# Kernel tuning notes

Measured on AMD Instinct MI355X. Metric: run time of the kernel, lower is better.

Reference implementation:

```python
import jax, jax.numpy as jnp
import numpy as np

B, C, T, HEADS = 4, 1024, 1024, 16


def setup_inputs() -> dict:
    key = jax.random.key(0)
    k0, k1, k2, k3 = jax.random.split(key, 4)
    x = jax.random.normal(k0, (B, C, T), dtype=jnp.float32)
    mask = jax.random.randint(k1, (B, T), 0, 2).astype(bool)  # True = masked position
    scale = 1.0 / np.sqrt(C).astype(np.float32)
    w_kvq = jax.random.normal(k2, (3 * C, C), dtype=jnp.float32) * scale  # Conv1d k=1, no bias
    w_out = jax.random.normal(k3, (C, C), dtype=jnp.float32) * scale
    return {"x": x, "mask": mask, "w_kvq": w_kvq, "w_out": w_out}


def reference(x, mask, w_kvq, w_out):
    b, c, t = x.shape
    h = HEADS
    d = c // h  # head dim; torch scales by sqrt(k.size(1)) = sqrt(d)
    # Conv1d with kernel 1 == per-timestep matmul over channels
    kvq = jnp.einsum('oc,bct->bot', w_kvq, x)  # [B, 3C, T]
    k, v, q = jnp.split(kvq, 3, axis=1)        # each [B, C, T]
    k = k.reshape(b, h, d, t)
    v = v.reshape(b, h, d, t)
    q = q.reshape(b, h, d, t)
    # att[b,h,i,j] = <k_i, q_j> / sqrt(d); i = key pos, j = query pos
    att = jnp.einsum('bhdi,bhdj->bhij', k, q) / jnp.sqrt(jnp.asarray(d, x.dtype))
    # pre-softmax: mask key positions (dim i) with -inf
    att = jnp.where(mask[:, None, :, None], -jnp.inf, att)
    att = jax.nn.softmax(att, axis=2)  # softmax over keys (torch dim=1 of [Bh,Tk,Tq])
    # post-softmax: zero out masked query positions (dim j)
    att = jnp.where(mask[:, None, None, :], jnp.asarray(0.0, x.dtype), att)
    o = jnp.einsum('bhdi,bhij->bhdj', v, att)  # [B, h, d, T]
    o = o.reshape(b, c, t)
    out = x + jnp.einsum('oc,bct->bot', w_out, o)
    # match torch layout: cat over heads along batch dim -> [h*B, T, T]
    att_flat = jnp.transpose(att, (1, 0, 2, 3)).reshape(h * b, t, t)
    return out, att_flat
```

## Files before the change

### kernel.cpp

```cpp
#include <hip/hip_runtime.h>

#define BB 4
#define CC 1024
#define TT 1024
#define HH 16
#define DD 64

typedef __bf16 v8bf __attribute__((ext_vector_type(8)));
typedef __bf16 v4bf __attribute__((ext_vector_type(4)));
typedef float  v4f  __attribute__((ext_vector_type(4)));

__device__ __forceinline__ void async16(const __bf16* g, __bf16* l) {
  __builtin_amdgcn_global_load_lds(
      (const __attribute__((address_space(1))) void*)g,
      (__attribute__((address_space(3))) void*)l, 16, 0, 0);
}

__global__ __launch_bounds__(256) void prep(
    const void* mraw, float* __restrict__ maskf, unsigned int* __restrict__ kmb,
    const float* __restrict__ w_kvq, const float* __restrict__ w_out,
    __bf16* __restrict__ wkb, __bf16* __restrict__ wob,
    const float* __restrict__ x, __bf16* __restrict__ xT)
{
  const int blk = blockIdx.x;
  const int tid = threadIdx.x;
  __shared__ int flagA, flagB;
  __shared__ __bf16 T[64][72];

  if (blk == 0) {
    if (tid == 0) { flagA = 0; flagB = 0; }
    __syncthreads();
    const unsigned char* mb = (const unsigned char*)mraw;
    const int n = BB * TT;
    int a = 0, bfl = 0;
    for (int i = tid; i < n; i += 256) {
      if (mb[i]) { if ((i & 3) == 0) a = 1; else bfl = 1; }
    }
    if (a)   atomicOr(&flagA, 1);
    if (bfl) atomicOr(&flagB, 1);
    __syncthreads();
    int layout;
    if (flagA && !flagB)      layout = 0;
    else if (!flagA && flagB) layout = 1;
    else                      layout = 2;
    const int lane = tid & 63, wave = tid >> 6;
    for (int it = 0; it < 16; it++) {
      int i = it * 256 + tid;
      float m;
      if (layout == 0)      m = (((const int*)mraw)[i]   != 0)   ? 1.f : 0.f;
      else if (layout == 1) m = (((const float*)mraw)[i] != 0.f) ? 1.f : 0.f;
      else                  m = (mb[i] != 0)                     ? 1.f : 0.f;
      maskf[i] = m;
      unsigned long long bal = __ballot(m != 0.f);
      if (lane == 0) {
        int base = (it * 256 + wave * 64) >> 5;
        kmb[base]     = (unsigned int)bal;
        kmb[base + 1] = (unsigned int)(bal >> 32);
      }
    }
  } else if (blk <= 2048) {
    const int cb = blk - 1;
    const float* src; __bf16* dst; int base;
    if (cb < 1536) { src = w_kvq; dst = wkb; base = cb * 2048; }
    else           { src = w_out; dst = wob; base = (cb - 1536) * 2048; }
    int i = base + tid * 8;
    float4 f0 = *(const float4*)(src + i);
    float4 f1 = *(const float4*)(src + i + 4);
    v8bf o;
    o[0] = (__bf16)f0.x; o[1] = (__bf16)f0.y; o[2] = (__bf16)f0.z; o[3] = (__bf16)f0.w;
    o[4] = (__bf16)f1.x; o[5] = (__bf16)f1.y; o[6] = (__bf16)f1.z; o[7] = (__bf16)f1.w;
    *(v8bf*)(dst + i) = o;
  } else {
    const int idx = blk - 2049;
    const int t0 = (idx & 15) * 64, c0 = ((idx >> 4) & 15) * 64, b = idx >> 8;
    {
      int row = tid >> 2, coff = (tid & 3) * 16;
      const float* src = x + ((long)b * CC + c0 + row) * TT + t0 + coff;
#pragma unroll
      for (int s = 0; s < 4; s++) {
        float4 f = *(const float4*)(src + s * 4);
        T[row][coff + s * 4 + 0] = (__bf16)f.x;
        T[row][coff + s * 4 + 1] = (__bf16)f.y;
        T[row][coff + s * 4 + 2] = (__bf16)f.z;
        T[row][coff + s * 4 + 3] = (__bf16)f.w;
      }
    }
    __syncthreads();
    {
      int trow = tid >> 2, ccoff = (tid & 3) * 16;
      __bf16 vals[16];
#pragma unroll
      for (int i = 0; i < 16; i++) vals[i] = T[ccoff + i][trow];
      __bf16* dst = xT + ((long)b * TT + t0 + trow) * CC + c0 + ccoff;
      *(v8bf*)dst       = *(v8bf*)&vals[0];
      *(v8bf*)(dst + 8) = *(v8bf*)&vals[8];
    }
  }
}

__global__ __launch_bounds__(256) void transpose_kq(const __bf16* __restrict__ kvqb,
                                                    __bf16* __restrict__ kqT) {
  const int zz = blockIdx.z;
  const int b = zz >> 1, part = zz & 1;
  const int srcbase = part == 0 ? 0 : 2 * CC;
  const int dstbase = part * CC;
  const int t0 = blockIdx.x * 64, c0 = blockIdx.y * 64;
  __shared__ __bf16 T[64][72];
  const int tid = threadIdx.x;
  {
    int row = tid >> 2, coff = (tid & 3) * 16;
    const __bf16* src = kvqb + ((long)b * 3 * CC + srcbase + c0 + row) * TT + t0 + coff;
    *(v8bf*)&T[row][coff]     = *(const v8bf*)src;
    *(v8bf*)&T[row][coff + 8] = *(const v8bf*)(src + 8);
  }
  __syncthreads();
  {
    int trow = tid >> 2, ccoff = (tid & 3) * 16;
    __bf16 vals[16];
#pragma unroll
    for (int i = 0; i < 16; i++) vals[i] = T[ccoff + i][trow];
    __bf16* dst = kqT + ((long)b * TT + t0 + trow) * (2 * CC) + dstbase + c0 + ccoff;
    *(v8bf*)dst       = *(v8bf*)&vals[0];
    *(v8bf*)(dst + 8) = *(v8bf*)&vals[8];
  }
}

template <int MODE, int NB, int MB>
__global__ __launch_bounds__(256) void gemm_bt(
    const __bf16* __restrict__ A, const __bf16* __restrict__ BTfull,
    const float* __restrict__ Sfull, void* __restrict__ Ofull,
    long strideBT, long strideOS)
{
  constexpr int TOT = NB * MB * BB;
  int flat = blockIdx.x + NB * (blockIdx.y + MB * blockIdx.z);
  int L = (flat & 7) * (TOT / 8) + (flat >> 3);
  const int n0 = (L % NB) * 128;
  const int m0 = ((L / NB) % MB) * 128;
  const int zb = L / (NB * MB);
  const __bf16* BT = BTfull + (long)zb * strideBT;
  __shared__ __align__(16) __bf16 As[128 * 32];
  __shared__ __align__(16) __bf16 Bs[128 * 32];
  const int tid = threadIdx.x;
  const int lane = tid & 63, wave = tid >> 6;
  const int wm = wave >> 1, wn = wave & 1;
  const int ln = lane & 15, q = lane >> 4;

  v4f acc[4][4];
#pragma unroll
  for (int i = 0; i < 4; i++)
#pragma unroll
    for (int j = 0; j < 4; j++) acc[i][j] = (v4f)(0.f);

  const int e0 = tid * 8;
  const int r0 = e0 >> 5, c0 = e0 & 31;
  const int e1 = (256 + tid) * 8;
  const int r1 = e1 >> 5, c1 = e1 & 31;
  const __bf16* ga0 = A  + (long)(m0 + r0) * CC + c0;
  const __bf16* ga1 = A  + (long)(m0 + r1) * CC + c1;
  const __bf16* gb0 = BT + (long)(n0 + r0) * CC + c0;
  const __bf16* gb1 = BT + (long)(n0 + r1) * CC + c1;
  __bf16* lA0 = &As[wave * 512];
  __bf16* lA1 = &As[2048 + wave * 512];
  __bf16* lB0 = &Bs[wave * 512];
  __bf16* lB1 = &Bs[2048 + wave * 512];

  for (int k0 = 0; k0 < CC; k0 += 32) {
    async16(ga0 + k0, lA0);
    async16(ga1 + k0, lA1);
    async16(gb0 + k0, lB0);
    async16(gb1 + k0, lB1);
    __syncthreads();
    v8bf af[4], bfr[4];
#pragma unroll
    for (int mi = 0; mi < 4; mi++)
      af[mi] = *(v8bf*)&As[(wm * 64 + mi * 16 + ln) * 32 + q * 8];
#pragma unroll
    for (int ni = 0; ni < 4; ni++)
      bfr[ni] = *(v8bf*)&Bs[(wn * 64 + ni * 16 + ln) * 32 + q * 8];
#pragma unroll
    for (int mi = 0; mi < 4; mi++)
#pragma unroll
      for (int ni = 0; ni < 4; ni++)
        acc[mi][ni] = __builtin_amdgcn_mfma_f32_16x16x32_bf16(af[mi], bfr[ni], acc[mi][ni], 0, 0, 0);
    __syncthreads();
  }
#pragma unroll
  for (int mi = 0; mi < 4; mi++)
#pragma unroll
    for (int ni = 0; ni < 4; ni++)
#pragma unroll
      for (int r = 0; r < 4; r++) {
        int row = m0 + wm * 64 + mi * 16 + q * 4 + r;
        int col = n0 + wn * 64 + ni * 16 + ln;
        if (MODE == 0) {
          ((__bf16*)Ofull)[(long)zb * strideOS + (long)row * TT + col] = (__bf16)acc[mi][ni][r];
        } else {
          long off = (long)zb * strideOS + (long)row * TT + col;
          ((float*)Ofull)[off] = acc[mi][ni][r] + Sfull[off];
        }
      }
}

__global__ __launch_bounds__(256) void attn_stats(
    const __bf16* __restrict__ kqT, const float* __restrict__ maskf,
    float* __restrict__ psum)
{
  int L = blockIdx.x + 8 * (blockIdx.y + 8 * blockIdx.z);
  L = (L & 7) * 512 + (L >> 3);
  const int jx = L & 7, iy = (L >> 3) & 7, z = L >> 6;
  const int h = z >> 2, b = z & 3;
  const int i0 = iy * 128, j0 = jx * 128;
  const __bf16* kbase = kqT + (long)b * TT * (2 * CC);
  const int tid = threadIdx.x;
  const int lane = tid & 63, wave = tid >> 6;
  const int wi = wave >> 1, wj = wave & 1;
  const int ln = lane & 15, q = lane >> 4;

  v8bf ak[4][2], bq[4][2];
#pragma unroll
  for (int mi = 0; mi < 4; mi++) {
    const __bf16* ar = kbase + (long)(i0 + wi * 64 + mi * 16 + ln) * (2 * CC) + h * DD;
    ak[mi][0] = *(const v8bf*)(ar + q * 8);
    ak[mi][1] = *(const v8bf*)(ar + 32 + q * 8);
  }
#pragma unroll
  for (int ni = 0; ni < 4; ni++) {
    const __bf16* br = kbase + (long)(j0 + wj * 64 + ni * 16 + ln) * (2 * CC) + CC + h * DD;
    bq[ni][0] = *(const v8bf*)(br + q * 8);
    bq[ni][1] = *(const v8bf*)(br + 32 + q * 8);
  }

  v4f acc[4][4];
  __builtin_amdgcn_s_setprio(1);
#pragma unroll
  for (int mi = 0; mi < 4; mi++)
#pragma unroll
    for (int ni = 0; ni < 4; ni++) {
      v4f a = (v4f)(0.f);
      a = __builtin_amdgcn_mfma_f32_16x16x32_bf16(ak[mi][0], bq[ni][0], a, 0, 0, 0);
      a = __builtin_amdgcn_mfma_f32_16x16x32_bf16(ak[mi][1], bq[ni][1], a, 0, 0, 0);
      acc[mi][ni] = a;
    }
  __builtin_amdgcn_s_setprio(0);

  float kmv[4][4];
#pragma unroll
  for (int mi = 0; mi < 4; mi++)
#pragma unroll
    for (int r = 0; r < 4; r++)
      kmv[mi][r] = maskf[b * TT + i0 + wi * 64 + mi * 16 + q * 4 + r];

#pragma unroll
  for (int ni = 0; ni < 4; ni++) {
    float s = 0.f;
#pragma unroll
    for (int mi = 0; mi < 4; mi++)
#pragma unroll
      for (int r = 0; r < 4; r++) {
        float e = (kmv[mi][r] != 0.f) ? 0.f : __expf(acc[mi][ni][r] * 0.125f);
        s += e;
      }
    s += __shfl_xor(s, 16, 64);
    s += __shfl_xor(s, 32, 64);
    if (q == 0) {
      long so = ((long)z * 16 + (i0 >> 6) + wi) * TT + j0 + wj * 64 + ni * 16 + ln;
      psum[so] = s;
    }
  }
}

__global__ __launch_bounds__(256) void gemm_pv(
    const __bf16* __restrict__ kqT, const __bf16* __restrict__ kvqb,
    const float* __restrict__ psum, const float* __restrict__ maskf,
    const unsigned int* __restrict__ kmb,
    float* __restrict__ att, __bf16* __restrict__ oT)
{
  int L = blockIdx.x + 16 * blockIdx.y;
  L = (L & 7) * 128 + (L >> 3);
  const int z = L >> 4, jb = L & 15;
  const int h = z >> 2, b = z & 3;
  const int j0 = jb * 64;
  __shared__ __align__(16) char smem[37376];
  float* stl = (float*)smem;
  unsigned int* kmw = (unsigned int*)(smem + 256);
  const int tid = threadIdx.x;
  const int lane = tid & 63, wave = tid >> 6;
  const int ln = lane & 15, q = lane >> 4;
  __bf16 (*Pt)[72] = (__bf16(*)[72])(smem + 512 + wave * 9216);

  const __bf16* kbase = kqT + (long)b * TT * (2 * CC);
  const __bf16* vbase = kvqb + (long)(b * 3 * CC + CC + h * DD) * TT;

  if (tid < 64) {
    float S = 0.f;
#pragma unroll
    for (int t = 0; t < 16; t++) S += psum[((long)z * 16 + t) * TT + j0 + tid];
    stl[tid] = (maskf[b * TT + j0 + tid] != 0.f) ? 0.f : 1.f / S;
  }
  if (tid < 32) kmw[tid] = kmb[b * 32 + tid];
  __syncthreads();

  v8bf bq[4][2];
#pragma unroll
  for (int ni = 0; ni < 4; ni++) {
    const __bf16* qr = kbase + (long)(j0 + ni * 16 + ln) * (2 * CC) + CC + h * DD;
    bq[ni][0] = *(const v8bf*)(qr + q * 8);
    bq[ni][1] = *(const v8bf*)(qr + 32 + q * 8);
  }
  float stq[4];
#pragma unroll
  for (int ni = 0; ni < 4; ni++) stq[ni] = stl[ni * 16 + ln];

  v4f acc[4][4];
#pragma unroll
  for (int i = 0; i < 4; i++)
#pragma unroll
    for (int j = 0; j < 4; j++) acc[i][j] = (v4f)(0.f);

  for (int it = 0; it < 4; it++) {
    const int ibase = wave * 256 + it * 64;
#pragma unroll
    for (int mi = 0; mi < 4; mi++) {
      const __bf16* arow = kbase + (long)(ibase + mi * 16 + ln) * (2 * CC) + h * DD;
      v8bf ak0 = *(const v8bf*)(arow + q * 8);
      v8bf ak1 = *(const v8bf*)(arow + 32 + q * 8);
#pragma unroll
      for (int ni = 0; ni < 4; ni++) {
        v4f l4 = (v4f)(0.f);
        l4 = __builtin_amdgcn_mfma_f32_16x16x32_bf16(ak0, bq[ni][0], l4, 0, 0, 0);
        l4 = __builtin_amdgcn_mfma_f32_16x16x32_bf16(ak1, bq[ni][1], l4, 0, 0, 0);
        v4bf pb;
#pragma unroll
        for (int r = 0; r < 4; r++) {
          int i_loc = mi * 16 + q * 4 + r;
          int i_glob = ibase + i_loc;
          unsigned int mbit = (kmw[i_glob >> 5] >> (i_glob & 31)) & 1u;
          float p = mbit ? 0.f : __expf(l4[r] * 0.125f) * stq[ni];
          att[((long)z << 20) + (long)i_glob * TT + j0 + ni * 16 + ln] = p;
          pb[r] = (__bf16)p;
        }
        *(v4bf*)&Pt[ni * 16 + ln][mi * 16 + q * 4] = pb;
      }
    }
    v8bf ap[4][2], bv[4][2];
#pragma unroll
    for (int ji = 0; ji < 4; ji++)
#pragma unroll
      for (int ki = 0; ki < 2; ki++)
        ap[ji][ki] = *(v8bf*)&Pt[ji * 16 + ln][ki * 32 + q * 8];
#pragma unroll
    for (int di = 0; di < 4; di++)
#pragma unroll
      for (int ki = 0; ki < 2; ki++)
        bv[di][ki] = *(const v8bf*)(vbase + (long)(di * 16 + ln) * TT + ibase + ki * 32 + q * 8);
    __builtin_amdgcn_s_setprio(1);
#pragma unroll
    for (int ji = 0; ji < 4; ji++)
#pragma unroll
      for (int di = 0; di < 4; di++) {
        acc[ji][di] = __builtin_amdgcn_mfma_f32_16x16x32_bf16(ap[ji][0], bv[di][0], acc[ji][di], 0, 0, 0);
        acc[ji][di] = __builtin_amdgcn_mfma_f32_16x16x32_bf16(ap[ji][1], bv[di][1], acc[ji][di], 0, 0, 0);
      }
    __builtin_amdgcn_s_setprio(0);
  }

  float (*red0)[68] = (float(*)[68])(smem + 512);
  float (*red1)[68] = (float(*)[68])(smem + 512 + 17408);
  __syncthreads();
  if ((wave & 1) == 0) {
    float (*red)[68] = (wave == 0) ? red0 : red1;
#pragma unroll
    for (int ji = 0; ji < 4; ji++)
#pragma unroll
      for (int di = 0; di < 4; di++)
#pragma unroll
        for (int r = 0; r < 4; r++)
          red[ji * 16 + q * 4 + r][di * 16 + ln] = acc[ji][di][r];
  }
  __syncthreads();
  if ((wave & 1) == 1) {
    float (*red)[68] = (wave == 1) ? red0 : red1;
#pragma unroll
    for (int ji = 0; ji < 4; ji++)
#pragma unroll
      for (int di = 0; di < 4; di++)
#pragma unroll
        for (int r = 0; r < 4; r++)
          red[ji * 16 + q * 4 + r][di * 16 + ln] += acc[ji][di][r];
  }
  __syncthreads();
  {
    int row = tid >> 2, c0 = (tid & 3) * 16;
    __bf16 ob[16];
#pragma unroll
    for (int i = 0; i < 16; i++) ob[i] = (__bf16)(red0[row][c0 + i] + red1[row][c0 + i]);
    __bf16* dst = oT + ((long)b * TT + j0 + row) * CC + h * DD + c0;
    *(v8bf*)dst       = *(v8bf*)&ob[0];
    *(v8bf*)(dst + 8) = *(v8bf*)&ob[8];
  }
}

extern "C" void kernel_launch(void* const* d_in, const int* in_sizes, int n_in,
                              void* d_out, int out_size, void* d_ws, size_t ws_size,
                              hipStream_t stream) {
  const float* x     = (const float*)d_in[0];
  const void*  mask  = d_in[1];
  const float* w_kvq = (const float*)d_in[2];
  const float* w_out = (const float*)d_in[3];

  float* out = (float*)d_out;
  float* att = out + (long)BB * CC * TT;

  char* wsb = (char*)d_ws;
  float*   maskf = (float*)(wsb + 0);
  __bf16*  wkb   = (__bf16*)(wsb + 16384);
  __bf16*  wob   = (__bf16*)(wsb + 6307840);
  __bf16*  xT    = (__bf16*)(wsb + 8404992);
  __bf16*  kqT   = (__bf16*)(wsb + 8404992);
  __bf16*  kvqb  = (__bf16*)(wsb + 25182208);
  __bf16*  oT    = (__bf16*)(wsb + 50348032);
  float*   psum  = (float*)(wsb + 58736640);
  unsigned int* kmb = (unsigned int*)(wsb + 62930944);

  prep<<<3073, 256, 0, stream>>>(mask, maskf, kmb, w_kvq, w_out, wkb, wob, x, xT);
  gemm_bt<0, 8, 24><<<dim3(8, 24, BB), 256, 0, stream>>>(
      wkb, xT, nullptr, kvqb, (long)CC * TT, (long)3 * CC * TT);
  transpose_kq<<<dim3(16, 16, 2 * BB), 256, 0, stream>>>(kvqb, kqT);
  attn_stats<<<dim3(8, 8, HH * BB), 256, 0, stream>>>(kqT, maskf, psum);
  gemm_pv<<<dim3(16, HH * BB), 256, 0, stream>>>(kqT, kvqb, psum, maskf, kmb, att, oT);
  gemm_bt<1, 8, 8><<<dim3(8, 8, BB), 256, 0, stream>>>(
      wob, oT, x, out, (long)CC * TT, (long)CC * TT);
}
```

Baseline: 462.1 us.

## Fuse K/Q transpose into projection GEMM epilogue and drop transpose kernel

The KVQ projection GEMM now writes K and Q tiles directly in transposed [T, 2C] layout through an LDS staging buffer, while V keeps the original layout. This removes the separate transpose_kq kernel launch along with its extra global read and write of K and Q. The new epilogue adds LDS traffic and barriers, and the kqT buffer moves to a new workspace offset. gemm_pv also gains a launch-bounds occupancy hint of 4 blocks per CU, which may constrain register allocation.

```diff
diff --git a/kernel.cpp b/kernel.cpp
--- a/kernel.cpp
+++ b/kernel.cpp
@@ -98,37 +98,11 @@
   }
 }
 
-__global__ __launch_bounds__(256) void transpose_kq(const __bf16* __restrict__ kvqb,
-                                                    __bf16* __restrict__ kqT) {
-  const int zz = blockIdx.z;
-  const int b = zz >> 1, part = zz & 1;
-  const int srcbase = part == 0 ? 0 : 2 * CC;
-  const int dstbase = part * CC;
-  const int t0 = blockIdx.x * 64, c0 = blockIdx.y * 64;
-  __shared__ __bf16 T[64][72];
-  const int tid = threadIdx.x;
-  {
-    int row = tid >> 2, coff = (tid & 3) * 16;
-    const __bf16* src = kvqb + ((long)b * 3 * CC + srcbase + c0 + row) * TT + t0 + coff;
-    *(v8bf*)&T[row][coff]     = *(const v8bf*)src;
-    *(v8bf*)&T[row][coff + 8] = *(const v8bf*)(src + 8);
-  }
-  __syncthreads();
-  {
-    int trow = tid >> 2, ccoff = (tid & 3) * 16;
-    __bf16 vals[16];
-#pragma unroll
-    for (int i = 0; i < 16; i++) vals[i] = T[ccoff + i][trow];
-    __bf16* dst = kqT + ((long)b * TT + t0 + trow) * (2 * CC) + dstbase + c0 + ccoff;
-    *(v8bf*)dst       = *(v8bf*)&vals[0];
-    *(v8bf*)(dst + 8) = *(v8bf*)&vals[8];
-  }
-}
-
 template <int MODE, int NB, int MB>
 __global__ __launch_bounds__(256) void gemm_bt(
     const __bf16* __restrict__ A, const __bf16* __restrict__ BTfull,
     const float* __restrict__ Sfull, void* __restrict__ Ofull,
+    __bf16* __restrict__ kqT_out,
     long strideBT, long strideOS)
 {
   constexpr int TOT = NB * MB * BB;
@@ -184,21 +158,66 @@
         acc[mi][ni] = __builtin_amdgcn_mfma_f32_16x16x32_bf16(af[mi], bfr[ni], acc[mi][ni], 0, 0, 0);
     __syncthreads();
   }
-#pragma unroll
-  for (int mi = 0; mi < 4; mi++)
-#pragma unroll
-    for (int ni = 0; ni < 4; ni++)
-#pragma unroll
-      for (int r = 0; r < 4; r++) {
-        int row = m0 + wm * 64 + mi * 16 + q * 4 + r;
-        int col = n0 + wn * 64 + ni * 16 + ln;
-        if (MODE == 0) {
-          ((__bf16*)Ofull)[(long)zb * strideOS + (long)row * TT + col] = (__bf16)acc[mi][ni][r];
-        } else {
+
+  if constexpr (MODE == 0) {
+    const int mb = m0 >> 7;
+    if (mb >= 8 && mb < 16) {
+#pragma unroll
+      for (int mi = 0; mi < 4; mi++)
+#pragma unroll
+        for (int ni = 0; ni < 4; ni++)
+#pragma unroll
+          for (int r = 0; r < 4; r++) {
+            int row = m0 + wm * 64 + mi * 16 + q * 4 + r;
+            int col = n0 + wn * 64 + ni * 16 + ln;
+            ((__bf16*)Ofull)[(long)zb * strideOS + (long)row * TT + col] = (__bf16)acc[mi][ni][r];
+          }
+    } else {
+      __shared__ __align__(16) __bf16 Tt[128][72];
+      const int cbase = (mb < 8) ? m0 : (m0 - 1024);
+      __bf16* dstb = kqT_out + (long)zb * TT * (2 * CC);
+#pragma unroll
+      for (int ph = 0; ph < 2; ph++) {
+        if (wm == ph) {
+#pragma unroll
+          for (int mi = 0; mi < 4; mi++)
+#pragma unroll
+            for (int ni = 0; ni < 4; ni++) {
+              v4bf pb;
+#pragma unroll
+              for (int r = 0; r < 4; r++) pb[r] = (__bf16)acc[mi][ni][r];
+              *(v4bf*)&Tt[wn * 64 + ni * 16 + ln][mi * 16 + q * 4] = pb;
+            }
+        }
+        __syncthreads();
+        {
+          int row = tid & 127, half = tid >> 7;
+          v8bf x0 = *(v8bf*)&Tt[row][half * 32];
+          v8bf x1 = *(v8bf*)&Tt[row][half * 32 + 8];
+          v8bf x2 = *(v8bf*)&Tt[row][half * 32 + 16];
+          v8bf x3 = *(v8bf*)&Tt[row][half * 32 + 24];
+          __bf16* d = dstb + (long)(n0 + row) * (2 * CC) + cbase + ph * 64 + half * 32;
+          *(v8bf*)(d)      = x0;
+          *(v8bf*)(d + 8)  = x1;
+          *(v8bf*)(d + 16) = x2;
+          *(v8bf*)(d + 24) = x3;
+        }
+        __syncthreads();
+      }
+    }
+  } else {
+#pragma unroll
+    for (int mi = 0; mi < 4; mi++)
+#pragma unroll
+      for (int ni = 0; ni < 4; ni++)
+#pragma unroll
+        for (int r = 0; r < 4; r++) {
+          int row = m0 + wm * 64 + mi * 16 + q * 4 + r;
+          int col = n0 + wn * 64 + ni * 16 + ln;
           long off = (long)zb * strideOS + (long)row * TT + col;
           ((float*)Ofull)[off] = acc[mi][ni][r] + Sfull[off];
         }
-      }
+  }
 }
 
 __global__ __launch_bounds__(256) void attn_stats(
@@ -269,7 +288,7 @@
   }
 }
 
-__global__ __launch_bounds__(256) void gemm_pv(
+__global__ __launch_bounds__(256, 4) void gemm_pv(
     const __bf16* __restrict__ kqT, const __bf16* __restrict__ kvqb,
     const float* __restrict__ psum, const float* __restrict__ maskf,
     const unsigned int* __restrict__ kmb,
@@ -424,10 +443,12 @@
 
   prep<<<3073, 256, 0, stream>>>(mask, maskf, kmb, w_kvq, w_out, wkb, wob, x, xT);
   gemm_bt<0, 8, 24><<<dim3(8, 24, BB), 256, 0, stream>>>(
-      wkb, xT, nullptr, kvqb, (long)CC * TT, (long)3 * CC * TT);
-  transpose_kq<<<dim3(16, 16, 2 * BB), 256, 0, stream>>>(kvqb, kqT);
-  attn_stats<<<dim3(8, 8, HH * BB), 256, 0, stream>>>(kqT, maskf, psum);
-  gemm_pv<<<dim3(16, HH * BB), 256, 0, stream>>>(kqT, kvqb, psum, maskf, kmb, att, oT);
+      wkb, xT, nullptr, kvqb, (__bf16*)(wsb + 67125248) ,
+      (long)CC * TT, (long)3 * CC * TT);
+  attn_stats<<<dim3(8, 8, HH * BB), 256, 0, stream>>>(
+      (const __bf16*)(wsb + 67125248), maskf, psum);
+  gemm_pv<<<dim3(16, HH * BB), 256, 0, stream>>>(
+      (const __bf16*)(wsb + 67125248), kvqb, psum, maskf, kmb, att, oT);
   gemm_bt<1, 8, 8><<<dim3(8, 8, BB), 256, 0, stream>>>(
-      wob, oT, x, out, (long)CC * TT, (long)CC * TT);
-}
+      wob, oT, x, out, nullptr, (long)CC * TT, (long)CC * TT);
+}
```

Result: slower. 607.3 us (+31.4%).
